# Performance work log

Measured on AMD Instinct MI355X. Metric: run time of the kernel, lower is better.

Reference implementation:

```python
import jax, jax.numpy as jnp
import numpy as np

D, H, DFF = 1024, 16, 4096
HD = D // H
NEG = -1e9  # finite stand-in for -inf causal mask (grad-safe)


def layer_norm(x, g, b, eps=1e-5):
    mu = jnp.mean(x, axis=-1, keepdims=True)
    var = jnp.mean(jnp.square(x - mu), axis=-1, keepdims=True)
    return (x - mu) * jax.lax.rsqrt(var + eps) * g + b


def setup_inputs() -> dict:
    key = jax.random.key(0)
    ks = jax.random.split(key, 16)
    B, T = 2, 2048
    x = jax.random.normal(ks[0], (B, T, D), jnp.float32)
    causal_mask = jnp.where(jnp.triu(jnp.ones((T, T), bool), k=1), NEG, 0.0).astype(jnp.float32)
    ema_attn = jax.random.uniform(ks[1], (H, T, T), jnp.float32)
    # normalize EMA rows like attention weights would be
    ema_attn = ema_attn / jnp.sum(ema_attn, axis=-1, keepdims=True)
    s = 0.02
    p = {
        'x': x, 'causal_mask': causal_mask, 'ema_attn': ema_attn,
        'log_tau_attn': jnp.array(0.0, jnp.float32),
        'Wq': jax.random.normal(ks[2], (D, D), jnp.float32) * s,
        'bq': jnp.zeros((D,), jnp.float32),
        'Wk': jax.random.normal(ks[3], (D, D), jnp.float32) * s,
        'bk': jnp.zeros((D,), jnp.float32),
        'Wv': jax.random.normal(ks[4], (D, D), jnp.float32) * s,
        'bv': jnp.zeros((D,), jnp.float32),
        'Wo': jax.random.normal(ks[5], (D, D), jnp.float32) * s,
        'bo': jnp.zeros((D,), jnp.float32),
        'W1': jax.random.normal(ks[6], (DFF, D), jnp.float32) * s,
        'b1': jnp.zeros((DFF,), jnp.float32),
        'W2': jax.random.normal(ks[7], (D, DFF), jnp.float32) * s,
        'b2': jnp.zeros((D,), jnp.float32),
        'g1': jnp.ones((D,), jnp.float32), 'beta1': jnp.zeros((D,), jnp.float32),
        'g2': jnp.ones((D,), jnp.float32), 'beta2': jnp.zeros((D,), jnp.float32),
    }
    return p


def reference(x, causal_mask, ema_attn, log_tau_attn, Wq, bq, Wk, bk, Wv, bv,
              Wo, bo, W1, b1, W2, b2, g1, beta1, g2, beta2):
    B, T, _ = x.shape
    # habituation bias: -tau_a * mean over heads of the EMA attention
    tau_a = jnp.exp(log_tau_attn)
    habit_bias = -(tau_a * ema_attn).mean(0)            # (T, T)
    attn_mask = causal_mask + habit_bias                # (T, T)

    # multi-head self-attention (torch MHA math, dropout=0 / eval)
    q = (x @ Wq.T + bq).reshape(B, T, H, HD)
    k = (x @ Wk.T + bk).reshape(B, T, H, HD)
    v = (x @ Wv.T + bv).reshape(B, T, H, HD)
    scores = jnp.einsum('bthd,bshd->bhts', q, k) / jnp.sqrt(jnp.float32(HD))
    scores = scores + attn_mask[None, None]             # (B, H, T, T)
    attn = jax.nn.softmax(scores, axis=-1)
    ctx = jnp.einsum('bhts,bshd->bthd', attn, v).reshape(B, T, D)
    attn_out = ctx @ Wo.T + bo

    # residual + norm, then FFN (GELU), residual + norm
    h = layer_norm(x + attn_out, g1, beta1)
    ff = (jax.nn.gelu(h @ W1.T + b1) @ W2.T) + b2
    out = layer_norm(h + ff, g2, beta2)
    return out
```

## Files before the change

### kernel.cpp

```cpp
#include <hip/hip_runtime.h>
#include <hip/hip_bf16.h>
#include <math.h>

#define T_SEQ 2048
#define D_MODEL 1024
#define BT 4096

typedef __bf16 bf16;
typedef __bf16 bf16x8 __attribute__((ext_vector_type(8)));
typedef __bf16 bf16x4 __attribute__((ext_vector_type(4)));
typedef float f32x4 __attribute__((ext_vector_type(4)));

__device__ __forceinline__ void gload_lds16(const bf16* g, bf16* l) {
  __builtin_amdgcn_global_load_lds(
      (__attribute__((address_space(1))) void*)(g),
      (__attribute__((address_space(3))) void*)(l), 16, 0, 0);
}

__global__ __launch_bounds__(256) void k_mask(const float* __restrict__ causal,
                                              const float* __restrict__ ema,
                                              const float* __restrict__ logtau,
                                              bf16* __restrict__ mask) {
  const int qt = blockIdx.x, st = blockIdx.y;
  if (st > qt) return;
  const int t = threadIdx.x;
  const float c = -__expf(logtau[0]) * (1.0f / 16.0f);
  const int r0 = t >> 4;
  const int cc = t & 15;
#pragma unroll
  for (int rr = 0; rr < 4; ++rr) {
    const size_t q = (size_t)qt * 64 + r0 + rr * 16;
    const size_t f4 = q * 512 + st * 16 + cc;
    float4 v = ((const float4*)causal)[f4];
    float a0 = v.x, a1 = v.y, a2 = v.z, a3 = v.w;
#pragma unroll
    for (int h = 0; h < 16; ++h) {
      float4 e = ((const float4*)(ema + (size_t)h * T_SEQ * T_SEQ))[f4];
      a0 += c * e.x; a1 += c * e.y; a2 += c * e.z; a3 += c * e.w;
    }
    bf16x4 o;
    o[0] = (bf16)a0; o[1] = (bf16)a1; o[2] = (bf16)a2; o[3] = (bf16)a3;
    ((bf16x4*)mask)[f4] = o;
  }
}

struct CvtArgs {
  const float* src[7];
  bf16* dst[7];
  int cum[8];
};
__global__ __launch_bounds__(256) void k_cvt_all(CvtArgs a) {
  const int i = blockIdx.x * 256 + threadIdx.x;
  if (i >= a.cum[7]) return;
  int s = 0;
#pragma unroll
  for (int k = 1; k < 7; ++k) s += (i >= a.cum[k]);
  const int j = i - a.cum[s];
  float4 v = ((const float4*)a.src[s])[j];
  bf16x4 o;
  o[0] = (bf16)v.x; o[1] = (bf16)v.y; o[2] = (bf16)v.z; o[3] = (bf16)v.w;
  ((bf16x4*)a.dst[s])[j] = o;
}

__global__ void k_bias3(const float* __restrict__ bq, const float* __restrict__ bk,
                        const float* __restrict__ bv, float* __restrict__ o) {
  const int i = blockIdx.x * 256 + threadIdx.x;
  o[i] = (i < 1024) ? bq[i] : (i < 2048 ? bk[i - 1024] : bv[i - 2048]);
}

__device__ __forceinline__ float gelu_tanh(float x) {
  return 0.5f * x * (1.0f + tanhf(0.7978845608028654f * (x + 0.044715f * x * x * x)));
}

template <int EPI>
__global__ __launch_bounds__(512, 2) void k_gemm_big(const bf16* __restrict__ A,
                                                     const bf16* __restrict__ B,
                                                     const float* __restrict__ bias,
                                                     const float* __restrict__ resid,
                                                     float* __restrict__ outf,
                                                     bf16* __restrict__ outb,
                                                     int K, int N) {
  __shared__ bf16 sA[2][256 * 64];
  __shared__ bf16 sB[2][256 * 64];
  const int tid = threadIdx.x;
  const int m0 = blockIdx.x * 256, n0 = blockIdx.y * 256;
  const int lane = tid & 63;
  const int w = tid >> 6, wr = w >> 2, wc = w & 3;
  const int lr = lane & 15, lg = lane >> 4;

  const int srow = lane >> 3;
  const int schunk = (lane & 7) ^ srow;

  auto stage = [&](int buf, int kt) {
    const int k0 = kt << 6;
#pragma unroll
    for (int e = 0; e < 4; ++e) {
      const int r = w * 32 + e * 8 + srow;
      gload_lds16(A + (size_t)(m0 + r) * K + k0 + schunk * 8,
                  &sA[buf][(w * 32 + e * 8) * 64 + lane * 8]);
      gload_lds16(B + (size_t)(n0 + r) * K + k0 + schunk * 8,
                  &sB[buf][(w * 32 + e * 8) * 64 + lane * 8]);
    }
  };

  f32x4 acc[8][4] = {};

  stage(0, 0);
  stage(1, 1);

  const int KT = K >> 6;
  for (int t = 0; t < KT; ++t) {
    if (t < KT - 1) asm volatile("s_waitcnt vmcnt(8)" ::: "memory");
    else            asm volatile("s_waitcnt vmcnt(0)" ::: "memory");
    __builtin_amdgcn_s_barrier();

    const int buf = t & 1;
    const char* pA = (const char*)sA[buf];
    const char* pB = (const char*)sB[buf];

    bf16x8 a0[8], b0[4];
#pragma unroll
    for (int m = 0; m < 8; ++m) {
      const int row = wr * 128 + m * 16 + lr;
      a0[m] = *(const bf16x8*)(pA + (unsigned)(row * 128) +
                               (((unsigned)lg) ^ (unsigned)(row & 7)) * 16u);
    }
#pragma unroll
    for (int n = 0; n < 4; ++n) {
      const int row = wc * 64 + n * 16 + lr;
      b0[n] = *(const bf16x8*)(pB + (unsigned)(row * 128) +
                               (((unsigned)lg) ^ (unsigned)(row & 7)) * 16u);
    }
    __builtin_amdgcn_s_setprio(1);
#pragma unroll
    for (int m = 0; m < 8; ++m)
#pragma unroll
      for (int n = 0; n < 4; ++n)
        acc[m][n] = __builtin_amdgcn_mfma_f32_16x16x32_bf16(a0[m], b0[n], acc[m][n], 0, 0, 0);
    __builtin_amdgcn_s_setprio(0);

    bf16x8 a1[8], b1[4];
#pragma unroll
    for (int m = 0; m < 8; ++m) {
      const int row = wr * 128 + m * 16 + lr;
      a1[m] = *(const bf16x8*)(pA + (unsigned)(row * 128) +
                               (((unsigned)(4 | lg)) ^ (unsigned)(row & 7)) * 16u);
    }
#pragma unroll
    for (int n = 0; n < 4; ++n) {
      const int row = wc * 64 + n * 16 + lr;
      b1[n] = *(const bf16x8*)(pB + (unsigned)(row * 128) +
                               (((unsigned)(4 | lg)) ^ (unsigned)(row & 7)) * 16u);
    }
    asm volatile("s_waitcnt lgkmcnt(0)" ::: "memory");
    __builtin_amdgcn_s_barrier();
    if (t + 2 < KT) stage(buf, t + 2);

    __builtin_amdgcn_s_setprio(1);
#pragma unroll
    for (int m = 0; m < 8; ++m)
#pragma unroll
      for (int n = 0; n < 4; ++n)
        acc[m][n] = __builtin_amdgcn_mfma_f32_16x16x32_bf16(a1[m], b1[n], acc[m][n], 0, 0, 0);
    __builtin_amdgcn_s_setprio(0);
  }

  const int row0 = m0 + wr * 128 + (lane >> 4) * 4;
  const int col0 = n0 + wc * 64 + lr;
#pragma unroll
  for (int m = 0; m < 8; ++m) {
#pragma unroll
    for (int n = 0; n < 4; ++n) {
      const int col = col0 + n * 16;
      const float bv = bias[col];
#pragma unroll
      for (int r = 0; r < 4; ++r) {
        const int row = row0 + m * 16 + r;
        float v = acc[m][n][r] + bv;
        if (EPI == 0) {
          outb[(size_t)row * N + col] = (bf16)v;
        } else if (EPI == 1) {
          v += resid[(size_t)row * N + col];
          outf[(size_t)row * N + col] = v;
        } else {
          outb[(size_t)row * N + col] = (bf16)gelu_tanh(v);
        }
      }
    }
  }
}

template <int EPI>
__global__ __launch_bounds__(256, 2) void k_gemm_ring2(const bf16* __restrict__ A,
                                                       const bf16* __restrict__ B,
                                                       const float* __restrict__ bias,
                                                       const float* __restrict__ resid,
                                                       float* __restrict__ outf,
                                                       bf16* __restrict__ outb,
                                                       int K, int N) {
  __shared__ bf16 sA[2][128 * 64];
  __shared__ bf16 sB[2][128 * 64];
  const int tid = threadIdx.x;
  const int m0 = blockIdx.x * 128, n0 = blockIdx.y * 128;
  const int lane = tid & 63;
  const int w = tid >> 6, wr = w >> 1, wc = w & 1;
  const int lr = lane & 15, lg = lane >> 4;

  const int srow = lane >> 3;
  const int schunk = (lane & 7) ^ srow;

  auto stage = [&](int buf, int kt) {
    const int k0 = kt << 6;
#pragma unroll
    for (int e = 0; e < 4; ++e) {
      const int r = w * 32 + e * 8 + srow;
      gload_lds16(A + (size_t)(m0 + r) * K + k0 + schunk * 8,
                  &sA[buf][(w * 32 + e * 8) * 64 + lane * 8]);
      gload_lds16(B + (size_t)(n0 + r) * K + k0 + schunk * 8,
                  &sB[buf][(w * 32 + e * 8) * 64 + lane * 8]);
    }
  };

  f32x4 acc[4][4] = {};

  stage(0, 0);
  stage(1, 1);

  const int KT = K >> 6;
  for (int t = 0; t < KT; ++t) {
    if (t < KT - 1) asm volatile("s_waitcnt vmcnt(8)" ::: "memory");
    else            asm volatile("s_waitcnt vmcnt(0)" ::: "memory");
    __builtin_amdgcn_s_barrier();

    const int buf = t & 1;
    const char* pA = (const char*)sA[buf];
    const char* pB = (const char*)sB[buf];
    bf16x8 af[4][2], bfr[4][2];
#pragma unroll
    for (int m = 0; m < 4; ++m) {
      const int row = wr * 64 + m * 16 + lr;
#pragma unroll
      for (int kk = 0; kk < 2; ++kk) {
        const unsigned off =
            (unsigned)(row * 128) + (((unsigned)((kk << 2) | lg)) ^ (unsigned)(row & 7)) * 16u;
        af[m][kk] = *(const bf16x8*)(pA + off);
      }
    }
#pragma unroll
    for (int n = 0; n < 4; ++n) {
      const int row = wc * 64 + n * 16 + lr;
#pragma unroll
      for (int kk = 0; kk < 2; ++kk) {
        const unsigned off =
            (unsigned)(row * 128) + (((unsigned)((kk << 2) | lg)) ^ (unsigned)(row & 7)) * 16u;
        bfr[n][kk] = *(const bf16x8*)(pB + off);
      }
    }
    asm volatile("s_waitcnt lgkmcnt(0)" ::: "memory");
    __builtin_amdgcn_s_barrier();
    if (t + 2 < KT) stage(buf, t + 2);

    __builtin_amdgcn_s_setprio(1);
#pragma unroll
    for (int m = 0; m < 4; ++m)
#pragma unroll
      for (int n = 0; n < 4; ++n)
#pragma unroll
        for (int kk = 0; kk < 2; ++kk)
          acc[m][n] = __builtin_amdgcn_mfma_f32_16x16x32_bf16(af[m][kk], bfr[n][kk],
                                                              acc[m][n], 0, 0, 0);
    __builtin_amdgcn_s_setprio(0);
  }

  const int row0 = m0 + wr * 64 + (lane >> 4) * 4;
  const int col0 = n0 + wc * 64 + lr;
#pragma unroll
  for (int m = 0; m < 4; ++m) {
#pragma unroll
    for (int n = 0; n < 4; ++n) {
      const int col = col0 + n * 16;
      const float bv = bias[col];
#pragma unroll
      for (int r = 0; r < 4; ++r) {
        const int row = row0 + m * 16 + r;
        float v = acc[m][n][r] + bv;
        if (EPI == 0) {
          outb[(size_t)row * N + col] = (bf16)v;
        } else if (EPI == 1) {
          v += resid[(size_t)row * N + col];
          outf[(size_t)row * N + col] = v;
        } else {
          outb[(size_t)row * N + col] = (bf16)gelu_tanh(v);
        }
      }
    }
  }
}

__global__ __launch_bounds__(256) void k_attn(const bf16* __restrict__ qkv,
                                              const bf16* __restrict__ maskb,
                                              bf16* __restrict__ ctx) {
  const int bh = blockIdx.x;
  const int qt = blockIdx.y;
  const int b = bh >> 4, h = bh & 15;
  const int tid = threadIdx.x, w = tid >> 6, lane = tid & 63;
  const int lr = lane & 15, lg = lane >> 4;

  __shared__ bf16 sK[2][64 * 64];
  __shared__ bf16 sVt[2][64 * 72];
  __shared__ bf16 sM[2][64 * 64];
  __shared__ bf16 sP[4][16 * 64];

  const size_t rs = 3072;
  const bf16* base = qkv + (size_t)b * T_SEQ * rs + h * 64;
  const int q0b = qt * 64;
  const int qrow = w * 16 + lr;

  bf16x8 qf[2];
#pragma unroll
  for (int kk = 0; kk < 2; ++kk) {
    bf16x8 q = *(const bf16x8*)(base + (size_t)(q0b + qrow) * rs + kk * 32 + lg * 8);
#pragma unroll
    for (int j = 0; j < 8; ++j) qf[kk][j] = (bf16)((float)q[j] * 0.125f);
  }

  const int srow = lane >> 3;
  const int scol = lane & 7;

  auto issueKM = [&](int s0, bf16* sKb, bf16* sMb) {
#pragma unroll
    for (int e = 0; e < 2; ++e) {
      const int kb = w * 16 + e * 8;
      const int r = kb + srow;
      const int cs = 8 * (scol ^ (r & 7));
      gload_lds16(base + (size_t)(s0 + r) * rs + 1024 + cs, &sKb[kb * 64 + lane * 8]);
      gload_lds16(maskb + (size_t)(q0b + r) * T_SEQ + s0 + cs, &sMb[kb * 64 + lane * 8]);
    }
  };
  auto loadV = [&](int s0, bf16x8 vv[2]) {
#pragma unroll
    for (int t = 0; t < 2; ++t) {
      const int c = w * 64 + lane + t * 256;
      vv[t] = *(const bf16x8*)(base + (size_t)(s0 + (c >> 3)) * rs + 2048 + (c & 7) * 8);
    }
  };
  auto writeV = [&](const bf16x8 vv[2], bf16* sVtb) {
    char* pb = (char*)sVtb;
#pragma unroll
    for (int t = 0; t < 2; ++t) {
      const int c = w * 64 + lane + t * 256;
      const int s = c >> 3, dc = c & 7;
#pragma unroll
      for (int j = 0; j < 8; ++j) {
        const unsigned ba = ((unsigned)((dc * 8 + j) * 72 + s) * 2) ^ ((unsigned)dc << 4);
        *(bf16*)(pb + ba) = vv[t][j];
      }
    }
  };

  float m_r = -3.0e38f, l_r = 0.0f;
  f32x4 o[4] = {};

  const float L2E = 1.44269504088896f;
  const int nt = qt + 1;
  const unsigned swzq = (unsigned)(lr & 7) << 4;

  {
    bf16x8 v0[2];
    loadV(0, v0);
    issueKM(0, sK[0], sM[0]);
    writeV(v0, sVt[0]);
  }
  __syncthreads();

  int cur = 0;
  for (int t = 0; t < nt; ++t, cur ^= 1) {
    const bool pf = (t + 1 < nt);
    bf16x8 vv[2];
    if (pf) {
      loadV((t + 1) * 64, vv);
      issueKM((t + 1) * 64, sK[cur ^ 1], sM[cur ^ 1]);
    }

    const char* sMc = (const char*)sM[cur];
    f32x4 sc[4];
#pragma unroll
    for (int n = 0; n < 4; ++n) {
      const unsigned ba = ((unsigned)(qrow * 128 + n * 32 + lg * 8)) ^ swzq;
      bf16x4 mk = *(const bf16x4*)(sMc + ba);
#pragma unroll
      for (int j = 0; j < 4; ++j) sc[n][j] = (float)mk[j];
    }

    const char* sKc = (const char*)sK[cur];
    __builtin_amdgcn_s_setprio(1);
#pragma unroll
    for (int n = 0; n < 4; ++n) {
      const int key = n * 16 + lr;
#pragma unroll
      for (int kk = 0; kk < 2; ++kk) {
        const unsigned boff =
            (unsigned)(key * 128 + kk * 64 + lg * 16) ^ ((unsigned)(key & 7) << 4);
        bf16x8 kf = *(const bf16x8*)(sKc + boff);
        sc[n] = __builtin_amdgcn_mfma_f32_16x16x32_bf16(kf, qf[kk], sc[n], 0, 0, 0);
      }
    }
    __builtin_amdgcn_s_setprio(0);

    float mx = -3.0e38f;
#pragma unroll
    for (int n = 0; n < 4; ++n)
#pragma unroll
      for (int j = 0; j < 4; ++j) mx = fmaxf(mx, sc[n][j]);
    mx = fmaxf(mx, __shfl_xor(mx, 16));
    mx = fmaxf(mx, __shfl_xor(mx, 32));

    if (!__all(mx <= m_r + 8.0f)) {
      const float mnew = fmaxf(m_r, mx);
      const float alpha = exp2f((m_r - mnew) * L2E);
      m_r = mnew;
      l_r *= alpha;
      float a4[4];
#pragma unroll
      for (int j = 0; j < 4; ++j) a4[j] = __shfl(alpha, (lane & 48) | (lg * 4 + j));
#pragma unroll
      for (int dt = 0; dt < 4; ++dt)
#pragma unroll
        for (int j = 0; j < 4; ++j) o[dt][j] *= a4[j];
    }

    const float mL2 = m_r * L2E;
    float ps = 0.0f;
    float pn[4][4];
#pragma unroll
    for (int n = 0; n < 4; ++n)
#pragma unroll
      for (int j = 0; j < 4; ++j) {
        const float p = exp2f(sc[n][j] * L2E - mL2);
        pn[n][j] = p;
        ps += p;
      }
    ps += __shfl_xor(ps, 16);
    ps += __shfl_xor(ps, 32);
    l_r += ps;

    if (pf) writeV(vv, sVt[cur ^ 1]);

    char* sPw = (char*)sP[w];
#pragma unroll
    for (int n = 0; n < 4; ++n) {
      bf16x4 pb;
#pragma unroll
      for (int j = 0; j < 4; ++j) pb[j] = (bf16)pn[n][j];
      *(bf16x4*)(sPw + (((unsigned)(lr * 128 + n * 32 + lg * 8)) ^ swzq)) = pb;
    }

    bf16x8 pa[2];
#pragma unroll
    for (int kk = 0; kk < 2; ++kk)
      pa[kk] = *(const bf16x8*)(sPw + (((unsigned)(lr * 128 + kk * 64 + lg * 16)) ^ swzq));
    const char* sVc = (const char*)sVt[cur];
    __builtin_amdgcn_s_setprio(1);
#pragma unroll
    for (int dt = 0; dt < 4; ++dt) {
      const int dd = dt * 16 + lr;
#pragma unroll
      for (int kk = 0; kk < 2; ++kk) {
        const unsigned ba =
            ((unsigned)(dd * 72 + kk * 32 + lg * 8) * 2) ^ ((unsigned)((dd >> 3) & 7) << 4);
        bf16x8 vb = *(const bf16x8*)(sVc + ba);
        o[dt] = __builtin_amdgcn_mfma_f32_16x16x32_bf16(pa[kk], vb, o[dt], 0, 0, 0);
      }
    }
    __builtin_amdgcn_s_setprio(0);
    __syncthreads();
  }

  float linv[4];
#pragma unroll
  for (int j = 0; j < 4; ++j) linv[j] = 1.0f / __shfl(l_r, (lane & 48) | (lg * 4 + j));
#pragma unroll
  for (int j = 0; j < 4; ++j) {
    const size_t row = (size_t)b * T_SEQ + q0b + w * 16 + lg * 4 + j;
#pragma unroll
    for (int dt = 0; dt < 4; ++dt)
      ctx[row * D_MODEL + h * 64 + dt * 16 + lr] = (bf16)(o[dt][j] * linv[j]);
  }
}

__global__ __launch_bounds__(256) void k_ln(const float* __restrict__ in,
                                            const float* __restrict__ g,
                                            const float* __restrict__ be,
                                            float* __restrict__ out,
                                            bf16* __restrict__ outb) {
  const int row = blockIdx.x, tid = threadIdx.x;
  const float4 v = *(const float4*)(in + (size_t)row * 1024 + tid * 4);
  float s = v.x + v.y + v.z + v.w;
  float s2 = v.x * v.x + v.y * v.y + v.z * v.z + v.w * v.w;
#pragma unroll
  for (int d = 1; d < 64; d <<= 1) { s += __shfl_xor(s, d); s2 += __shfl_xor(s2, d); }
  __shared__ float red[8];
  const int w = tid >> 6;
  if ((tid & 63) == 0) { red[w] = s; red[4 + w] = s2; }
  __syncthreads();
  s = red[0] + red[1] + red[2] + red[3];
  s2 = red[4] + red[5] + red[6] + red[7];
  const float mu = s * (1.0f / 1024.0f);
  const float var = s2 * (1.0f / 1024.0f) - mu * mu;
  const float inv = rsqrtf(var + 1e-5f);
  const int col = tid * 4;
  const float4 gv = *(const float4*)(g + col);
  const float4 bv = *(const float4*)(be + col);
  float4 y;
  y.x = (v.x - mu) * inv * gv.x + bv.x;
  y.y = (v.y - mu) * inv * gv.y + bv.y;
  y.z = (v.z - mu) * inv * gv.z + bv.z;
  y.w = (v.w - mu) * inv * gv.w + bv.w;
  *(float4*)(out + (size_t)row * 1024 + col) = y;
  if (outb) {
    bf16x4 ob;
    ob[0] = (bf16)y.x; ob[1] = (bf16)y.y; ob[2] = (bf16)y.z; ob[3] = (bf16)y.w;
    *(bf16x4*)(outb + (size_t)row * 1024 + col) = ob;
  }
}

extern "C" void kernel_launch(void* const* d_in, const int* in_sizes, int n_in,
                              void* d_out, int out_size, void* d_ws, size_t ws_size,
                              hipStream_t stream) {
  const float* x      = (const float*)d_in[0];
  const float* causal = (const float*)d_in[1];
  const float* ema    = (const float*)d_in[2];
  const float* logtau = (const float*)d_in[3];
  const float* Wq = (const float*)d_in[4];
  const float* bq = (const float*)d_in[5];
  const float* Wk = (const float*)d_in[6];
  const float* bk = (const float*)d_in[7];
  const float* Wv = (const float*)d_in[8];
  const float* bv = (const float*)d_in[9];
  const float* Wo = (const float*)d_in[10];
  const float* bo = (const float*)d_in[11];
  const float* W1 = (const float*)d_in[12];
  const float* b1 = (const float*)d_in[13];
  const float* W2 = (const float*)d_in[14];
  const float* b2 = (const float*)d_in[15];
  const float* g1  = (const float*)d_in[16];
  const float* be1 = (const float*)d_in[17];
  const float* g2  = (const float*)d_in[18];
  const float* be2 = (const float*)d_in[19];
  float* out = (float*)d_out;

  char* ws = (char*)d_ws;
  bf16*  maskb = (bf16*)(ws + 0);
  bf16*  x_bf  = (bf16*)(ws + (16UL << 20));
  bf16*  wqkv  = (bf16*)(ws + (24UL << 20));
  bf16*  wo_bf = (bf16*)(ws + (30UL << 20));
  bf16*  w1_bf = (bf16*)(ws + (32UL << 20));
  bf16*  w2_bf = (bf16*)(ws + (40UL << 20));
  float* bqkv  = (float*)(ws + (48UL << 20));
  bf16*  qkv   = (bf16*)(ws + (49UL << 20));
  bf16*  ctxb  = (bf16*)(ws + (73UL << 20));
  float* h_pre = (float*)(ws + (81UL << 20));
  float* hbuf  = (float*)(ws + (97UL << 20));
  bf16*  h_bf  = (bf16*)(ws + (113UL << 20));
  bf16*  ff1   = (bf16*)(ws + (121UL << 20));
  float* out_pre = (float*)(ws + 0);

  const dim3 blk(256);
  const dim3 blk512(512);

  k_mask<<<dim3(32, 32), blk, 0, stream>>>(causal, ema, logtau, maskb);

  CvtArgs ca;
  ca.src[0] = x;  ca.dst[0] = x_bf;
  ca.src[1] = Wq; ca.dst[1] = wqkv;
  ca.src[2] = Wk; ca.dst[2] = wqkv + (1UL << 20);
  ca.src[3] = Wv; ca.dst[3] = wqkv + (2UL << 20);
  ca.src[4] = Wo; ca.dst[4] = wo_bf;
  ca.src[5] = W1; ca.dst[5] = w1_bf;
  ca.src[6] = W2; ca.dst[6] = w2_bf;
  ca.cum[0] = 0;
  ca.cum[1] = 1048576;
  ca.cum[2] = 1048576 + 262144;
  ca.cum[3] = 1048576 + 524288;
  ca.cum[4] = 1048576 + 786432;
  ca.cum[5] = 2097152;
  ca.cum[6] = 2097152 + 1048576;
  ca.cum[7] = 4194304;
  k_cvt_all<<<dim3(16384), blk, 0, stream>>>(ca);
  k_bias3<<<dim3(12), blk, 0, stream>>>(bq, bk, bv, bqkv);

  k_gemm_big<0><<<dim3(16, 12), blk512, 0, stream>>>(x_bf, wqkv, bqkv, nullptr, nullptr,
                                                     qkv, 1024, 3072);

  k_attn<<<dim3(32, 32), blk, 0, stream>>>(qkv, maskb, ctxb);

  k_gemm_ring2<1><<<dim3(32, 8), blk, 0, stream>>>(ctxb, wo_bf, bo, x, h_pre, nullptr,
                                                   1024, 1024);

  k_ln<<<dim3(4096), blk, 0, stream>>>(h_pre, g1, be1, hbuf, h_bf);

  k_gemm_big<2><<<dim3(16, 16), blk512, 0, stream>>>(h_bf, w1_bf, b1, nullptr, nullptr,
                                                     ff1, 1024, 4096);

  k_gemm_ring2<1><<<dim3(32, 8), blk, 0, stream>>>(ff1, w2_bf, b2, hbuf, out_pre, nullptr,
                                                   4096, 1024);

  k_ln<<<dim3(4096), blk, 0, stream>>>(out_pre, g2, be2, out, nullptr);
}
```

Baseline: 321.4 us.

## Split-K the N=1024 GEMMs, fold residual into LayerNorm, read mask directly

The two N=1024 projection GEMMs (Wo and W2) now use a 2-way split-K over a z grid dimension, so 512 blocks are launched instead of 256. Each half writes an fp32 partial buffer, and a new k_ln3 kernel sums the two partials with the residual before normalising. This raises occupancy on the CUs for these small-N GEMMs at the cost of extra fp32 partial writes and reads. Separately, the attention kernel drops the LDS staging of the mask, loads mask values straight from global into registers and adds them after QK^T, and raises launch bounds to 3 blocks per CU to use the LDS freed.

```diff
diff --git a/kernel.cpp b/kernel.cpp
--- a/kernel.cpp
+++ b/kernel.cpp
@@ -190,18 +190,19 @@
   }
 }
 
-template <int EPI>
-__global__ __launch_bounds__(256, 2) void k_gemm_ring2(const bf16* __restrict__ A,
-                                                       const bf16* __restrict__ B,
-                                                       const float* __restrict__ bias,
-                                                       const float* __restrict__ resid,
-                                                       float* __restrict__ outf,
-                                                       bf16* __restrict__ outb,
-                                                       int K, int N) {
+__global__ __launch_bounds__(256, 2) void k_gemm_splitk(const bf16* __restrict__ A,
+                                                        const bf16* __restrict__ B,
+                                                        const float* __restrict__ bias,
+                                                        float* __restrict__ p0,
+                                                        float* __restrict__ p1,
+                                                        int K, int N, int Kc) {
   __shared__ bf16 sA[2][128 * 64];
   __shared__ bf16 sB[2][128 * 64];
   const int tid = threadIdx.x;
   const int m0 = blockIdx.x * 128, n0 = blockIdx.y * 128;
+  const int z = blockIdx.z;
+  const int kb = z * Kc;
+  float* __restrict__ po = z ? p1 : p0;
   const int lane = tid & 63;
   const int w = tid >> 6, wr = w >> 1, wc = w & 1;
   const int lr = lane & 15, lg = lane >> 4;
@@ -210,7 +211,7 @@
   const int schunk = (lane & 7) ^ srow;
 
   auto stage = [&](int buf, int kt) {
-    const int k0 = kt << 6;
+    const int k0 = kb + (kt << 6);
 #pragma unroll
     for (int e = 0; e < 4; ++e) {
       const int r = w * 32 + e * 8 + srow;
@@ -226,7 +227,7 @@
   stage(0, 0);
   stage(1, 1);
 
-  const int KT = K >> 6;
+  const int KT = Kc >> 6;
   for (int t = 0; t < KT; ++t) {
     if (t < KT - 1) asm volatile("s_waitcnt vmcnt(8)" ::: "memory");
     else            asm volatile("s_waitcnt vmcnt(0)" ::: "memory");
@@ -279,27 +280,19 @@
 #pragma unroll
     for (int n = 0; n < 4; ++n) {
       const int col = col0 + n * 16;
-      const float bv = bias[col];
+      const float bv = z ? 0.0f : bias[col];
 #pragma unroll
       for (int r = 0; r < 4; ++r) {
         const int row = row0 + m * 16 + r;
-        float v = acc[m][n][r] + bv;
-        if (EPI == 0) {
-          outb[(size_t)row * N + col] = (bf16)v;
-        } else if (EPI == 1) {
-          v += resid[(size_t)row * N + col];
-          outf[(size_t)row * N + col] = v;
-        } else {
-          outb[(size_t)row * N + col] = (bf16)gelu_tanh(v);
-        }
-      }
-    }
-  }
-}
-
-__global__ __launch_bounds__(256) void k_attn(const bf16* __restrict__ qkv,
-                                              const bf16* __restrict__ maskb,
-                                              bf16* __restrict__ ctx) {
+        po[(size_t)row * N + col] = acc[m][n][r] + bv;
+      }
+    }
+  }
+}
+
+__global__ __launch_bounds__(256, 3) void k_attn(const bf16* __restrict__ qkv,
+                                                 const bf16* __restrict__ maskb,
+                                                 bf16* __restrict__ ctx) {
   const int bh = blockIdx.x;
   const int qt = blockIdx.y;
   const int b = bh >> 4, h = bh & 15;
@@ -308,13 +301,13 @@
 
   __shared__ bf16 sK[2][64 * 64];
   __shared__ bf16 sVt[2][64 * 72];
-  __shared__ bf16 sM[2][64 * 64];
   __shared__ bf16 sP[4][16 * 64];
 
   const size_t rs = 3072;
   const bf16* base = qkv + (size_t)b * T_SEQ * rs + h * 64;
   const int q0b = qt * 64;
   const int qrow = w * 16 + lr;
+  const bf16* mrow = maskb + (size_t)(q0b + qrow) * T_SEQ;
 
   bf16x8 qf[2];
 #pragma unroll
@@ -327,14 +320,13 @@
   const int srow = lane >> 3;
   const int scol = lane & 7;
 
-  auto issueKM = [&](int s0, bf16* sKb, bf16* sMb) {
+  auto issueK = [&](int s0, bf16* sKb) {
 #pragma unroll
     for (int e = 0; e < 2; ++e) {
       const int kb = w * 16 + e * 8;
       const int r = kb + srow;
       const int cs = 8 * (scol ^ (r & 7));
       gload_lds16(base + (size_t)(s0 + r) * rs + 1024 + cs, &sKb[kb * 64 + lane * 8]);
-      gload_lds16(maskb + (size_t)(q0b + r) * T_SEQ + s0 + cs, &sMb[kb * 64 + lane * 8]);
     }
   };
   auto loadV = [&](int s0, bf16x8 vv[2]) {
@@ -368,7 +360,7 @@
   {
     bf16x8 v0[2];
     loadV(0, v0);
-    issueKM(0, sK[0], sM[0]);
+    issueK(0, sK[0]);
     writeV(v0, sVt[0]);
   }
   __syncthreads();
@@ -379,20 +371,16 @@
     bf16x8 vv[2];
     if (pf) {
       loadV((t + 1) * 64, vv);
-      issueKM((t + 1) * 64, sK[cur ^ 1], sM[cur ^ 1]);
-    }
-
-    const char* sMc = (const char*)sM[cur];
-    f32x4 sc[4];
-#pragma unroll
-    for (int n = 0; n < 4; ++n) {
-      const unsigned ba = ((unsigned)(qrow * 128 + n * 32 + lg * 8)) ^ swzq;
-      bf16x4 mk = *(const bf16x4*)(sMc + ba);
-#pragma unroll
-      for (int j = 0; j < 4; ++j) sc[n][j] = (float)mk[j];
-    }
+      issueK((t + 1) * 64, sK[cur ^ 1]);
+    }
+
+    bf16x4 mk[4];
+#pragma unroll
+    for (int n = 0; n < 4; ++n)
+      mk[n] = *(const bf16x4*)(mrow + t * 64 + n * 16 + lg * 4);
 
     const char* sKc = (const char*)sK[cur];
+    f32x4 sc[4] = {};
     __builtin_amdgcn_s_setprio(1);
 #pragma unroll
     for (int n = 0; n < 4; ++n) {
@@ -411,7 +399,10 @@
 #pragma unroll
     for (int n = 0; n < 4; ++n)
 #pragma unroll
-      for (int j = 0; j < 4; ++j) mx = fmaxf(mx, sc[n][j]);
+      for (int j = 0; j < 4; ++j) {
+        sc[n][j] += (float)mk[n][j];
+        mx = fmaxf(mx, sc[n][j]);
+      }
     mx = fmaxf(mx, __shfl_xor(mx, 16));
     mx = fmaxf(mx, __shfl_xor(mx, 32));
 
@@ -488,13 +479,23 @@
   }
 }
 
-__global__ __launch_bounds__(256) void k_ln(const float* __restrict__ in,
-                                            const float* __restrict__ g,
-                                            const float* __restrict__ be,
-                                            float* __restrict__ out,
-                                            bf16* __restrict__ outb) {
+__global__ __launch_bounds__(256) void k_ln3(const float* __restrict__ p0,
+                                             const float* __restrict__ p1,
+                                             const float* __restrict__ resid,
+                                             const float* __restrict__ g,
+                                             const float* __restrict__ be,
+                                             float* __restrict__ out,
+                                             bf16* __restrict__ outb) {
   const int row = blockIdx.x, tid = threadIdx.x;
-  const float4 v = *(const float4*)(in + (size_t)row * 1024 + tid * 4);
+  const size_t i4 = (size_t)row * 256 + tid;
+  const float4 a = ((const float4*)p0)[i4];
+  const float4 bq = ((const float4*)p1)[i4];
+  const float4 cr = ((const float4*)resid)[i4];
+  float4 v;
+  v.x = a.x + bq.x + cr.x;
+  v.y = a.y + bq.y + cr.y;
+  v.z = a.z + bq.z + cr.z;
+  v.w = a.w + bq.w + cr.w;
   float s = v.x + v.y + v.z + v.w;
   float s2 = v.x * v.x + v.y * v.y + v.z * v.z + v.w * v.w;
 #pragma unroll
@@ -559,11 +560,11 @@
   float* bqkv  = (float*)(ws + (48UL << 20));
   bf16*  qkv   = (bf16*)(ws + (49UL << 20));
   bf16*  ctxb  = (bf16*)(ws + (73UL << 20));
-  float* h_pre = (float*)(ws + (81UL << 20));
   float* hbuf  = (float*)(ws + (97UL << 20));
   bf16*  h_bf  = (bf16*)(ws + (113UL << 20));
   bf16*  ff1   = (bf16*)(ws + (121UL << 20));
-  float* out_pre = (float*)(ws + 0);
+  float* part0 = (float*)(ws + (49UL << 20));
+  float* part1 = (float*)(ws + 0);
 
   const dim3 blk(256);
   const dim3 blk512(512);
@@ -594,16 +595,16 @@
 
   k_attn<<<dim3(32, 32), blk, 0, stream>>>(qkv, maskb, ctxb);
 
-  k_gemm_ring2<1><<<dim3(32, 8), blk, 0, stream>>>(ctxb, wo_bf, bo, x, h_pre, nullptr,
-                                                   1024, 1024);
-
-  k_ln<<<dim3(4096), blk, 0, stream>>>(h_pre, g1, be1, hbuf, h_bf);
+  k_gemm_splitk<<<dim3(32, 8, 2), blk, 0, stream>>>(ctxb, wo_bf, bo, part0, part1,
+                                                    1024, 1024, 512);
+
+  k_ln3<<<dim3(4096), blk, 0, stream>>>(part0, part1, x, g1, be1, hbuf, h_bf);
 
   k_gemm_big<2><<<dim3(16, 16), blk512, 0, stream>>>(h_bf, w1_bf, b1, nullptr, nullptr,
                                                      ff1, 1024, 4096);
 
-  k_gemm_ring2<1><<<dim3(32, 8), blk, 0, stream>>>(ff1, w2_bf, b2, hbuf, out_pre, nullptr,
-                                                   4096, 1024);
-
-  k_ln<<<dim3(4096), blk, 0, stream>>>(out_pre, g2, be2, out, nullptr);
-}
+  k_gemm_splitk<<<dim3(32, 8, 2), blk, 0, stream>>>(ff1, w2_bf, b2, part0, part1,
+                                                    4096, 1024, 2048);
+
+  k_ln3<<<dim3(4096), blk, 0, stream>>>(part0, part1, hbuf, g2, be2, out, nullptr);
+}
```

Result: faster. 304.2 us (-5.3%).
